# Kernel optimization log

Hardware: AMD Instinct MI355X
Metric: run time of the kernel (lower is better)

Reference implementation:

```python
import jax, jax.numpy as jnp
import numpy as np

D = 32            # dims[0] == dims[1] (modes per register)
K = 8             # kernel_size (filter interferometer modes)
STRIDE = 8        # stride (== kernel_size -> block-diagonal register)
N_BLOCKS = (D - K) // STRIDE + 1          # filters per register = 4
N_PHI = K * (K - 1) // 2                  # Reck triangle: one Ry BS per crossing = 28
BATCH = 16


def _filter_unitary(phi):
    """K-mode Reck-triangle interferometer of BS.Ry(theta=-2*phi) gates.
    Each gate mixes adjacent modes (j-1, j) with the real rotation
    [[cos phi, sin phi], [-sin phi, cos phi]]. Returns real [K, K] orthogonal."""
    U = jnp.eye(K, dtype=phi.dtype)
    idx = 0
    for i in range(1, K):
        for j in range(i, 0, -1):
            c, s = jnp.cos(phi[idx]), jnp.sin(phi[idx])
            r0 = c * U[j - 1] + s * U[j]
            r1 = -s * U[j - 1] + c * U[j]
            U = U.at[j - 1].set(r0).at[j].set(r1)
            idx += 1
    return U


def _register_unitary(phi):
    """D-mode register: the SAME filter unitary (shared params) placed every
    STRIDE modes; identity on any leftover modes. Block-diagonal [D, D]."""
    uf = _filter_unitary(phi)
    U = jnp.eye(D, dtype=phi.dtype)
    for b in range(N_BLOCKS):
        o = b * STRIDE
        U = U.at[o:o + K, o:o + K].set(uf)
    return U


def setup_inputs() -> dict:
    key = jax.random.key(0)
    k1, k2, k3 = jax.random.split(key, 3)
    two_pi = jnp.float32(2.0 * np.pi)
    return {
        "rho": jax.random.normal(k1, (BATCH, D * D, D * D), dtype=jnp.float32),
        "phi_x": two_pi * jax.random.uniform(k2, (N_PHI,), dtype=jnp.float32),
        "phi_y": two_pi * jax.random.uniform(k3, (N_PHI,), dtype=jnp.float32),
    }


def reference(rho, phi_x, phi_y):
    # u = kron(u_x, u_y) : [D^2, D^2] real orthogonal (BS circuit => real)
    u = jnp.kron(_register_unitary(phi_x), _register_unitary(phi_y))
    # new_rho = u @ rho @ u^dagger ; real => dagger is transpose
    u_rho = jnp.einsum('ij,bjk->bik', u, rho)   # [b, D^2, D^2]
    return u_rho @ u.T
```

## Files before the change

kernel.cpp:

```cpp
#include <hip/hip_runtime.h>
#include <hip/hip_bf16.h>
#include <math.h>


__global__ void setup_uf(const float* __restrict__ phi_x,
                         const float* __restrict__ phi_y,
                         float* __restrict__ ws) {
    const int t = threadIdx.x;
    if (t < 2) {
        const float* phi = (t == 0) ? phi_x : phi_y;
        float U[8][8];
#pragma unroll
        for (int i = 0; i < 8; ++i)
#pragma unroll
            for (int j = 0; j < 8; ++j) U[i][j] = (i == j) ? 1.0f : 0.0f;
        int idx = 0;
#pragma unroll
        for (int i = 1; i < 8; ++i) {
#pragma unroll
            for (int j = i; j >= 1; --j) {
                const float c = cosf(phi[idx]);
                const float s = sinf(phi[idx]);
#pragma unroll
                for (int m = 0; m < 8; ++m) {
                    const float a = U[j - 1][m], b = U[j][m];
                    U[j - 1][m] = c * a + s * b;
                    U[j][m]     = -s * a + c * b;
                }
                ++idx;
            }
        }
        float* o = ws + t * 64;
#pragma unroll
        for (int i = 0; i < 8; ++i)
#pragma unroll
            for (int j = 0; j < 8; ++j) o[i * 8 + j] = U[i][j];
    }
}

#define CONTRACT_INNER(M, a)                                                   \
    _Pragma("unroll")                                                          \
    for (int _g = 0; _g < 8; ++_g) {                                           \
        float _tmp[8];                                                         \
        _Pragma("unroll")                                                      \
        for (int _i = 0; _i < 8; ++_i) {                                       \
            float _acc = 0.0f;                                                 \
            _Pragma("unroll")                                                  \
            for (int _k = 0; _k < 8; ++_k)                                     \
                _acc = fmaf((M)[_i * 8 + _k], (a)[_g * 8 + _k], _acc);         \
            _tmp[_i] = _acc;                                                   \
        }                                                                      \
        _Pragma("unroll")                                                      \
        for (int _i = 0; _i < 8; ++_i) (a)[_g * 8 + _i] = _tmp[_i];            \
    }

#define CONTRACT_OUTER(M, a)                                                   \
    _Pragma("unroll")                                                          \
    for (int _g = 0; _g < 8; ++_g) {                                           \
        float _tmp[8];                                                         \
        _Pragma("unroll")                                                      \
        for (int _i = 0; _i < 8; ++_i) {                                       \
            float _acc = 0.0f;                                                 \
            _Pragma("unroll")                                                  \
            for (int _k = 0; _k < 8; ++_k)                                     \
                _acc = fmaf((M)[_i * 8 + _k], (a)[_k * 8 + _g], _acc);         \
            _tmp[_i] = _acc;                                                   \
        }                                                                      \
        _Pragma("unroll")                                                      \
        for (int _i = 0; _i < 8; ++_i) (a)[_i * 8 + _g] = _tmp[_i];            \
    }

__global__ __launch_bounds__(256) void qconv_fused(const float* __restrict__ rho,
                                                   const float* __restrict__ ws,
                                                   float* __restrict__ out) {
    __shared__ __align__(16) unsigned short Sh[16384];
    const int t   = threadIdx.x;
    const int bid = blockIdx.x;
    const int bx2 = bid & 3;
    const int by1 = (bid >> 2) & 3;
    const int bx1 = (bid >> 4) & 3;
    const int b   = bid >> 6;

    const float* __restrict__ UX = ws;
    const float* __restrict__ UY = ws + 64;

    const size_t B0      = (size_t)b << 20;
    const int    rowbase = bx1 * 256 + by1 * 8;
    const int    cg      = bx2 * 256 + t;

    const float* __restrict__ src = rho + B0 + (size_t)rowbase * 1024 + cg;

    float v[64];
#pragma unroll
    for (int i = 0; i < 8; ++i)
#pragma unroll
        for (int j = 0; j < 8; ++j)
            v[i * 8 + j] = src[(size_t)(i * 32 + j) * 1024];

    CONTRACT_INNER(UY, v)
    CONTRACT_OUTER(UX, v)

    {
        const int sb = t >> 3;
        const int il = t & 7;
#pragma unroll
        for (int r = 0; r < 64; ++r) {
            const int slot = sb ^ ((r << 1) & 31);
            __hip_bfloat16 h = __float2bfloat16(v[r]);
            Sh[r * 256 + slot * 8 + il] = *reinterpret_cast<unsigned short*>(&h);
        }
    }
    __syncthreads();

    const int rr  = t >> 2;
    const int by2 = t & 3;
    const int rsw = (rr << 1) & 31;
    const unsigned short* __restrict__ Srow = Sh + rr * 256;

    float q[64];
#pragma unroll
    for (int x2 = 0; x2 < 8; ++x2) {
        const int slot = (x2 * 4 + by2) ^ rsw;
        const uint4 u = *reinterpret_cast<const uint4*>(Srow + slot * 8);
        float raw[8];
        raw[0] = __uint_as_float(u.x << 16);
        raw[1] = __uint_as_float(u.x & 0xffff0000u);
        raw[2] = __uint_as_float(u.y << 16);
        raw[3] = __uint_as_float(u.y & 0xffff0000u);
        raw[4] = __uint_as_float(u.z << 16);
        raw[5] = __uint_as_float(u.z & 0xffff0000u);
        raw[6] = __uint_as_float(u.w << 16);
        raw[7] = __uint_as_float(u.w & 0xffff0000u);

        float w8[8];
#pragma unroll
        for (int jj = 0; jj < 8; ++jj) {
            float a = 0.0f;
#pragma unroll
            for (int j = 0; j < 8; ++j)
                a = fmaf(UY[jj * 8 + j], raw[j], a);
            w8[jj] = a;
        }
#pragma unroll
        for (int xp = 0; xp < 8; ++xp) {
            const float ux = UX[xp * 8 + x2];
#pragma unroll
            for (int jj = 0; jj < 8; ++jj) {
                if (x2 == 0) q[xp * 8 + jj] = ux * w8[jj];
                else         q[xp * 8 + jj] = fmaf(ux, w8[jj], q[xp * 8 + jj]);
            }
        }
    }

    const int gr = rowbase + ((rr >> 3) * 32) + (rr & 7);
    float* __restrict__ dst = out + B0 + (size_t)gr * 1024 + bx2 * 256 + by2 * 8;
#pragma unroll
    for (int xp = 0; xp < 8; ++xp) {
        *reinterpret_cast<float4*>(dst + xp * 32) =
            make_float4(q[xp * 8 + 0], q[xp * 8 + 1], q[xp * 8 + 2], q[xp * 8 + 3]);
        *reinterpret_cast<float4*>(dst + xp * 32 + 4) =
            make_float4(q[xp * 8 + 4], q[xp * 8 + 5], q[xp * 8 + 6], q[xp * 8 + 7]);
    }
}

extern "C" void kernel_launch(void* const* d_in, const int* in_sizes, int n_in,
                              void* d_out, int out_size, void* d_ws, size_t ws_size,
                              hipStream_t stream) {
    const float* rho   = (const float*)d_in[0];
    const float* phi_x = (const float*)d_in[1];
    const float* phi_y = (const float*)d_in[2];
    float* out = (float*)d_out;
    float* ws  = (float*)d_ws;

    setup_uf<<<1, 64, 0, stream>>>(phi_x, phi_y, ws);
    qconv_fused<<<1024, 256, 0, stream>>>(rho, ws, out);
}
```

Baseline: 46.99 us.

## Split each tile's output x-rows across two blocks to double the grid

Each block now computes only half of the x1 output rows (4 of 8), so the grid doubles to 2048 blocks and per-thread register arrays and shared memory are halved. Loads are streamed per k with the UY contraction done immediately, and the UX contraction is accumulated into 32 outputs instead of 64. The aim is to cut register pressure, raise occupancy and expose more parallelism. The cost is that each block re-reads the full 8x8 input slab it needs, so global reads of rho double, and the second-stage thread mapping is changed.

```diff
diff --git a/kernel.cpp b/kernel.cpp
--- a/kernel.cpp
+++ b/kernel.cpp
@@ -38,48 +38,17 @@
     }
 }
 
-#define CONTRACT_INNER(M, a)                                                   \
-    _Pragma("unroll")                                                          \
-    for (int _g = 0; _g < 8; ++_g) {                                           \
-        float _tmp[8];                                                         \
-        _Pragma("unroll")                                                      \
-        for (int _i = 0; _i < 8; ++_i) {                                       \
-            float _acc = 0.0f;                                                 \
-            _Pragma("unroll")                                                  \
-            for (int _k = 0; _k < 8; ++_k)                                     \
-                _acc = fmaf((M)[_i * 8 + _k], (a)[_g * 8 + _k], _acc);         \
-            _tmp[_i] = _acc;                                                   \
-        }                                                                      \
-        _Pragma("unroll")                                                      \
-        for (int _i = 0; _i < 8; ++_i) (a)[_g * 8 + _i] = _tmp[_i];            \
-    }
-
-#define CONTRACT_OUTER(M, a)                                                   \
-    _Pragma("unroll")                                                          \
-    for (int _g = 0; _g < 8; ++_g) {                                           \
-        float _tmp[8];                                                         \
-        _Pragma("unroll")                                                      \
-        for (int _i = 0; _i < 8; ++_i) {                                       \
-            float _acc = 0.0f;                                                 \
-            _Pragma("unroll")                                                  \
-            for (int _k = 0; _k < 8; ++_k)                                     \
-                _acc = fmaf((M)[_i * 8 + _k], (a)[_k * 8 + _g], _acc);         \
-            _tmp[_i] = _acc;                                                   \
-        }                                                                      \
-        _Pragma("unroll")                                                      \
-        for (int _i = 0; _i < 8; ++_i) (a)[_i * 8 + _g] = _tmp[_i];            \
-    }
-
 __global__ __launch_bounds__(256) void qconv_fused(const float* __restrict__ rho,
                                                    const float* __restrict__ ws,
                                                    float* __restrict__ out) {
-    __shared__ __align__(16) unsigned short Sh[16384];
+    __shared__ __align__(16) unsigned short Sh[8192];
     const int t   = threadIdx.x;
     const int bid = blockIdx.x;
     const int bx2 = bid & 3;
     const int by1 = (bid >> 2) & 3;
     const int bx1 = (bid >> 4) & 3;
-    const int b   = bid >> 6;
+    const int x1h = (bid >> 6) & 1;
+    const int b   = bid >> 7;
 
     const float* __restrict__ UX = ws;
     const float* __restrict__ UY = ws + 64;
@@ -90,34 +59,52 @@
 
     const float* __restrict__ src = rho + B0 + (size_t)rowbase * 1024 + cg;
 
-    float v[64];
+    float acc[32];
 #pragma unroll
-    for (int i = 0; i < 8; ++i)
+    for (int k = 0; k < 8; ++k) {
+        float raw[8];
 #pragma unroll
         for (int j = 0; j < 8; ++j)
-            v[i * 8 + j] = src[(size_t)(i * 32 + j) * 1024];
-
-    CONTRACT_INNER(UY, v)
-    CONTRACT_OUTER(UX, v)
+            raw[j] = src[(size_t)(k * 32 + j) * 1024];
+        float w[8];
+#pragma unroll
+        for (int jj = 0; jj < 8; ++jj) {
+            float a = 0.0f;
+#pragma unroll
+            for (int j = 0; j < 8; ++j)
+                a = fmaf(UY[jj * 8 + j], raw[j], a);
+            w[jj] = a;
+        }
+#pragma unroll
+        for (int ii = 0; ii < 4; ++ii) {
+            const float ux = UX[(x1h * 4 + ii) * 8 + k];
+#pragma unroll
+            for (int jj = 0; jj < 8; ++jj) {
+                if (k == 0) acc[ii * 8 + jj] = ux * w[jj];
+                else        acc[ii * 8 + jj] = fmaf(ux, w[jj], acc[ii * 8 + jj]);
+            }
+        }
+    }
 
     {
         const int sb = t >> 3;
         const int il = t & 7;
 #pragma unroll
-        for (int r = 0; r < 64; ++r) {
+        for (int r = 0; r < 32; ++r) {
             const int slot = sb ^ ((r << 1) & 31);
-            __hip_bfloat16 h = __float2bfloat16(v[r]);
+            __hip_bfloat16 h = __float2bfloat16(acc[r]);
             Sh[r * 256 + slot * 8 + il] = *reinterpret_cast<unsigned short*>(&h);
         }
     }
     __syncthreads();
 
-    const int rr  = t >> 2;
-    const int by2 = t & 3;
+    const int rr  = t & 31;
+    const int by2 = (t >> 5) & 3;
+    const int x2h = t >> 7;
     const int rsw = (rr << 1) & 31;
     const unsigned short* __restrict__ Srow = Sh + rr * 256;
 
-    float q[64];
+    float q[32];
 #pragma unroll
     for (int x2 = 0; x2 < 8; ++x2) {
         const int slot = (x2 * 4 + by2) ^ rsw;
@@ -142,8 +129,8 @@
             w8[jj] = a;
         }
 #pragma unroll
-        for (int xp = 0; xp < 8; ++xp) {
-            const float ux = UX[xp * 8 + x2];
+        for (int xp = 0; xp < 4; ++xp) {
+            const float ux = UX[(x2h * 4 + xp) * 8 + x2];
 #pragma unroll
             for (int jj = 0; jj < 8; ++jj) {
                 if (x2 == 0) q[xp * 8 + jj] = ux * w8[jj];
@@ -152,10 +139,11 @@
         }
     }
 
-    const int gr = rowbase + ((rr >> 3) * 32) + (rr & 7);
-    float* __restrict__ dst = out + B0 + (size_t)gr * 1024 + bx2 * 256 + by2 * 8;
+    const int gr = rowbase + (x1h * 4 + (rr >> 3)) * 32 + (rr & 7);
+    float* __restrict__ dst =
+        out + B0 + (size_t)gr * 1024 + bx2 * 256 + x2h * 128 + by2 * 8;
 #pragma unroll
-    for (int xp = 0; xp < 8; ++xp) {
+    for (int xp = 0; xp < 4; ++xp) {
         *reinterpret_cast<float4*>(dst + xp * 32) =
             make_float4(q[xp * 8 + 0], q[xp * 8 + 1], q[xp * 8 + 2], q[xp * 8 + 3]);
         *reinterpret_cast<float4*>(dst + xp * 32 + 4) =
@@ -173,5 +161,5 @@
     float* ws  = (float*)d_ws;
 
     setup_uf<<<1, 64, 0, stream>>>(phi_x, phi_y, ws);
-    qconv_fused<<<1024, 256, 0, stream>>>(rho, ws, out);
+    qconv_fused<<<2048, 256, 0, stream>>>(rho, ws, out);
 }
```

Measured after the change: 47.16 us. About the same (+0.4%).
